# Kernel optimization log

Hardware: AMD Instinct MI355X
Metric: run time of the kernel (lower is better)

Reference implementation:

```python
import jax, jax.numpy as jnp
import numpy as np

NODELEN = 17949
N_NODES = 512
N_EDGES = 4096
H2 = 768
EMB = 128
IN_DIM = 2 * NODELEN


def _seg_mean(h, src, dst, n):
    # gather neighbor features and mean-reduce per destination node
    msg = h[src]                                   # [E, F]
    s = jax.ops.segment_sum(msg, dst, num_segments=n)
    deg = jax.ops.segment_sum(jnp.ones((src.shape[0],), h.dtype), dst, num_segments=n)
    return s / jnp.maximum(deg, 1.0)[:, None]


def setup_inputs() -> dict:
    key = jax.random.key(0)
    ks = jax.random.split(key, 12)
    s = 0.02
    return {
        "x": jax.random.normal(ks[0], (N_NODES, NODELEN), jnp.float32),
        "edge_src": jax.random.randint(ks[1], (N_EDGES,), 0, N_NODES),
        "edge_dst": jax.random.randint(ks[2], (N_EDGES,), 0, N_NODES),
        "W_e2": jax.random.normal(ks[3], (H2, IN_DIM), jnp.float32) * s,
        "b_e2": jnp.zeros((H2,), jnp.float32),
        "W_e3": jax.random.normal(ks[4], (EMB, H2), jnp.float32) * s,
        "b_e3": jnp.zeros((EMB,), jnp.float32),
        "W_d1": jax.random.normal(ks[5], (H2, EMB), jnp.float32) * s,
        "b_d1": jnp.zeros((H2,), jnp.float32),
        "W_d3": jax.random.normal(ks[6], (IN_DIM, H2), jnp.float32) * s,
        "b_d3": jnp.zeros((IN_DIM,), jnp.float32),
    }


def reference(x, edge_src, edge_dst, W_e2, b_e2, W_e3, b_e3, W_d1, b_d1, W_d3, b_d3):
    n = x.shape[0]
    # depth-2 recursive GraphSAGE mean aggregation; agg[0]=0 after each hop
    h1 = _seg_mean(x, edge_src, edge_dst, n).at[:, 0].set(0.0)
    h2 = _seg_mean(h1, edge_src, edge_dst, n).at[:, 0].set(0.0)
    emb = jnp.concatenate([x, h2], axis=1)           # [N, 2*NODELEN]
    emb = emb.at[:, 0].set(0.0).at[:, NODELEN].set(0.0)
    # AutoEncoder (eval mode: dropout is identity)
    h = jax.nn.relu(emb @ W_e2.T + b_e2)
    encoded = h @ W_e3.T + b_e3
    h = jax.nn.relu(encoded @ W_d1.T + b_d1)
    decoded = h @ W_d3.T + b_d3
    return encoded, decoded
```

## Files before the change

kernel.cpp:

```cpp
#include <hip/hip_runtime.h>
#include <hip/hip_bf16.h>

#define NODELEN 17949
#define NN 512
#define NE 4096
#define H2 768
#define EMB 128
#define IN_DIM (2 * NODELEN)
#define KP1 35904
#define KITERS1 561
#define SPLITS 24
#define KCHUNK1 24
#define FPAD 18048
#define RPAD4 35968

#define BM 128
#define BN 128
#define BK 64

typedef __bf16 bf16x8 __attribute__((ext_vector_type(8)));
typedef float f32x4 __attribute__((ext_vector_type(4)));

#define GPTR(p) ((const __attribute__((address_space(1))) void*)(p))
#define LPTR(p) ((__attribute__((address_space(3))) void*)(p))


__global__ void k_zero_int(int* p, int n) {
    int i = blockIdx.x * 256 + threadIdx.x;
    if (i < n) p[i] = 0;
}

__global__ void k_zero_f4(float4* p, int n4) {
    int i = blockIdx.x * 256 + threadIdx.x;
    if (i < n4) p[i] = make_float4(0.f, 0.f, 0.f, 0.f);
}

__global__ void k_deg(const int* __restrict__ dst, int* __restrict__ cnt) {
    int e = blockIdx.x * 256 + threadIdx.x;
    if (e < NE) atomicAdd(&cnt[dst[e]], 1);
}

__global__ void k_invdeg(const int* __restrict__ cnt, float* __restrict__ invdeg) {
    int i = blockIdx.x * 256 + threadIdx.x;
    if (i < NN) {
        int c = cnt[i];
        invdeg[i] = 1.0f / (float)(c > 1 ? c : 1);
    }
}

__global__ void k_scatter(const int* __restrict__ src, const int* __restrict__ dst,
                          const float* __restrict__ invdeg, float* __restrict__ A) {
    int e = blockIdx.x * 256 + threadIdx.x;
    if (e < NE) {
        int d = dst[e];
        atomicAdd(&A[(size_t)d * NN + src[e]], invdeg[d]);
    }
}

__global__ void k_a2(const float* __restrict__ A, __bf16* __restrict__ A2b) {
    int i = blockIdx.x;
    int t = threadIdx.x;
    __shared__ float row[NN];
    row[t] = A[(size_t)i * NN + t];
    row[t + 256] = A[(size_t)i * NN + 256 + t];
    __syncthreads();
    float a0 = 0.f, a1 = 0.f;
    for (int s = 0; s < NN; ++s) {
        float a = row[s];
        if (a != 0.f) {
            a0 += a * A[(size_t)s * NN + t];
            a1 += a * A[(size_t)s * NN + 256 + t];
        }
    }
    A2b[(size_t)i * NN + t] = (__bf16)a0;
    A2b[(size_t)i * NN + 256 + t] = (__bf16)a1;
}

__global__ void k_xt_emb(const float* __restrict__ x, __bf16* __restrict__ xT,
                         __bf16* __restrict__ embb) {
    __shared__ float t[64][65];
    int f0 = blockIdx.x * 64, s0 = blockIdx.y * 64;
    int tx = threadIdx.x & 63, ty = threadIdx.x >> 6;
#pragma unroll
    for (int r = 0; r < 16; ++r) {
        int f = f0 + tx;
        int s = s0 + ty * 16 + r;
        float v = (f < NODELEN) ? x[(size_t)s * NODELEN + f] : 0.f;
        t[ty * 16 + r][tx] = v;
        if (f < NODELEN)
            embb[(size_t)s * KP1 + f] = (__bf16)((f == 0) ? 0.f : v);
    }
    __syncthreads();
#pragma unroll
    for (int r = 0; r < 16; ++r) {
        int f = f0 + ty * 16 + r;
        if (f < FPAD) xT[(size_t)f * NN + s0 + tx] = (__bf16)t[tx][ty * 16 + r];
    }
}

__global__ void k_pad(__bf16* __restrict__ embb) {
    int i = blockIdx.x * 256 + threadIdx.x;
    const int PAD = KP1 - IN_DIM;
    if (i < NN * PAD) {
        int n = i / PAD, c = i % PAD;
        embb[(size_t)n * KP1 + IN_DIM + c] = (__bf16)0.f;
    }
}

__global__ void k_cvt(const float* __restrict__ src, __bf16* __restrict__ dst,
                      int R, int C, int Rpad, int Cpad) {
    int C8 = Cpad / 8;
    int idx = blockIdx.x * 256 + threadIdx.x;
    if (idx >= Rpad * C8) return;
    int r = idx / C8, c8 = (idx % C8) * 8;
    __align__(16) __bf16 o[8];
    if (r < R && c8 + 8 <= C) {
        const float2* p = (const float2*)(src + (size_t)r * C + c8);
#pragma unroll
        for (int j = 0; j < 4; ++j) {
            float2 f = p[j];
            o[2 * j] = (__bf16)f.x;
            o[2 * j + 1] = (__bf16)f.y;
        }
    } else {
#pragma unroll
        for (int j = 0; j < 8; ++j) {
            int c = c8 + j;
            o[j] = (r < R && c < C) ? (__bf16)src[(size_t)r * C + c] : (__bf16)0.f;
        }
    }
    *(uint4*)&dst[(size_t)r * Cpad + c8] = *(uint4*)o;
}


template <int EPI>
__global__ __launch_bounds__(256, 4) void gemm_k(
        const __bf16* __restrict__ A, int lda,
        const __bf16* __restrict__ B, int ldb,
        int Nvalid, int kIters, int kChunk,
        float* __restrict__ Cf, int ldc, const float* __restrict__ bias,
        __bf16* __restrict__ Cb) {
    __shared__ __align__(16) __bf16 As[BM * BK];
    __shared__ __align__(16) __bf16 Bs[BN * BK];

    const int tid = threadIdx.x;

    const int gx = gridDim.x, gy = gridDim.y;
    const int nwg = gx * gy * (int)gridDim.z;
    const int fid = blockIdx.x + gx * (blockIdx.y + gy * blockIdx.z);
    const int q = nwg >> 3, r = nwg & 7;
    const int xcd = fid & 7, idx = fid >> 3;
    const int lid = (xcd < r) ? xcd * (q + 1) + idx
                              : r * (q + 1) + (xcd - r) * q + idx;
    const int m0 = (lid % gx) * BM;
    const int rem = lid / gx;
    const int n0 = (rem % gy) * BN;
    const int z = rem / gy;

    int it0 = z * kChunk;
    int it1 = it0 + kChunk;
    if (it1 > kIters) it1 = kIters;

    const int wave = tid >> 6;
    const int lane = tid & 63;
    const int wm = (wave & 1) * 64;
    const int wn = (wave >> 1) * 64;
    const int fl = lane & 15;
    const int fq = lane >> 4;

    const __bf16* Abase = A + (size_t)(m0 + (tid >> 3)) * lda + (tid & 7) * 8;
    const __bf16* Bbase = B + (size_t)(n0 + (tid >> 3)) * ldb + (tid & 7) * 8;
    char* AsW = (char*)As + wave * 1024;
    char* BsW = (char*)Bs + wave * 1024;

    f32x4 acc[4][4] = {};

    for (int it = it0; it < it1; ++it) {
        const __bf16* Ag = Abase + it * BK;
        const __bf16* Bg = Bbase + it * BK;
#pragma unroll
        for (int rr = 0; rr < 4; ++rr)
            __builtin_amdgcn_global_load_lds(
                GPTR(Ag + (size_t)rr * 32 * lda), LPTR(AsW + rr * 4096), 16, 0, 0);
#pragma unroll
        for (int rr = 0; rr < 4; ++rr)
            __builtin_amdgcn_global_load_lds(
                GPTR(Bg + (size_t)rr * 32 * ldb), LPTR(BsW + rr * 4096), 16, 0, 0);
        __syncthreads();

#pragma unroll
        for (int ks = 0; ks < 2; ++ks) {
            const int kk = ks * 32 + fq * 8;
            bf16x8 af[4], bfr[4];
#pragma unroll
            for (int i = 0; i < 4; ++i)
                af[i] = *(const bf16x8*)&As[(wm + i * 16 + fl) * BK + kk];
#pragma unroll
            for (int j = 0; j < 4; ++j)
                bfr[j] = *(const bf16x8*)&Bs[(wn + j * 16 + fl) * BK + kk];
#pragma unroll
            for (int i = 0; i < 4; ++i)
#pragma unroll
                for (int j = 0; j < 4; ++j)
                    acc[i][j] = __builtin_amdgcn_mfma_f32_16x16x32_bf16(
                        af[i], bfr[j], acc[i][j], 0, 0, 0);
        }
        __syncthreads();
    }

#pragma unroll
    for (int i = 0; i < 4; ++i) {
#pragma unroll
        for (int j = 0; j < 4; ++j) {
#pragma unroll
            for (int rr = 0; rr < 4; ++rr) {
                int m = m0 + wm + i * 16 + fq * 4 + rr;
                int n = n0 + wn + j * 16 + fl;
                float v = acc[i][j][rr];
                if (EPI == 0) {
                    Cf[((size_t)z * NN + m) * H2 + n] = v;
                } else if (EPI == 1) {
                    if (n < Nvalid) Cf[(size_t)m * ldc + n] = v + bias[n];
                } else {
                    if (n < Nvalid)
                        Cb[(size_t)m * KP1 + NODELEN + n] = (n == 0) ? (__bf16)0.f : (__bf16)v;
                }
            }
        }
    }
}

__global__ void k_reduce(const float* __restrict__ partials,
                         const float* __restrict__ bias, float* __restrict__ h) {
    const int T4 = NN * H2 / 4;
    int i4 = blockIdx.x * 256 + threadIdx.x;
    if (i4 >= T4) return;
    const float4* p = (const float4*)partials;
    float4 s = make_float4(0.f, 0.f, 0.f, 0.f);
#pragma unroll
    for (int zz = 0; zz < SPLITS; ++zz) {
        float4 v = p[(size_t)zz * T4 + i4];
        s.x += v.x; s.y += v.y; s.z += v.z; s.w += v.w;
    }
    const float4 b = *(const float4*)&bias[(i4 * 4) % H2];
    s.x += b.x; s.y += b.y; s.z += b.z; s.w += b.w;
    s.x = s.x > 0.f ? s.x : 0.f;
    s.y = s.y > 0.f ? s.y : 0.f;
    s.z = s.z > 0.f ? s.z : 0.f;
    s.w = s.w > 0.f ? s.w : 0.f;
    *(float4*)&h[(size_t)i4 * 4] = s;
}

__global__ void k_enc(const float* __restrict__ h, const float* __restrict__ W,
                      const float* __restrict__ b, float* __restrict__ out) {
    int m = blockIdx.x, e = threadIdx.x;
    const float4* hr = (const float4*)(h + (size_t)m * H2);
    const float4* wr = (const float4*)(W + (size_t)e * H2);
    float s = 0.f;
#pragma unroll 4
    for (int i = 0; i < H2 / 4; ++i) {
        float4 a = hr[i];
        float4 w = wr[i];
        s += a.x * w.x + a.y * w.y + a.z * w.z + a.w * w.w;
    }
    out[(size_t)m * EMB + e] = s + b[e];
}

__global__ void k_dec1(const float* __restrict__ enc, const float* __restrict__ W,
                       const float* __restrict__ b, __bf16* __restrict__ hd) {
    int m = blockIdx.x;
    __shared__ float er[EMB];
    if (threadIdx.x < EMB) er[threadIdx.x] = enc[(size_t)m * EMB + threadIdx.x];
    __syncthreads();
    for (int j = threadIdx.x; j < H2; j += 256) {
        const float4* wr = (const float4*)(W + (size_t)j * EMB);
        float s = 0.f;
#pragma unroll
        for (int i = 0; i < EMB / 4; ++i) {
            float4 w = wr[i];
            s += w.x * er[4 * i] + w.y * er[4 * i + 1] + w.z * er[4 * i + 2] +
                 w.w * er[4 * i + 3];
        }
        float v = s + b[j];
        hd[(size_t)m * H2 + j] = (__bf16)(v > 0.f ? v : 0.f);
    }
}


extern "C" void kernel_launch(void* const* d_in, const int* in_sizes, int n_in,
                              void* d_out, int out_size, void* d_ws, size_t ws_size,
                              hipStream_t stream) {
    const float* x = (const float*)d_in[0];
    const int* esrc = (const int*)d_in[1];
    const int* edst = (const int*)d_in[2];
    const float* W_e2 = (const float*)d_in[3];
    const float* b_e2 = (const float*)d_in[4];
    const float* W_e3 = (const float*)d_in[5];
    const float* b_e3 = (const float*)d_in[6];
    const float* W_d1 = (const float*)d_in[7];
    const float* b_d1 = (const float*)d_in[8];
    const float* W_d3 = (const float*)d_in[9];
    const float* b_d3 = (const float*)d_in[10];
    float* out = (float*)d_out;

    char* w = (char*)d_ws;
    auto alloc = [&](size_t bytes) {
        char* p = w;
        w += (bytes + 255) & ~(size_t)255;
        return p;
    };
    __bf16* embb = (__bf16*)alloc((size_t)NN * KP1 * 2);
    char* uni = (char*)alloc((size_t)SPLITS * NN * H2 * 4);
    __bf16* xTb = (__bf16*)uni;
    float* Adj = (float*)(uni + (size_t)FPAD * NN * 2);
    __bf16* A2b = (__bf16*)((char*)Adj + (size_t)NN * NN * 4);
    int* cnt = (int*)((char*)A2b + (size_t)NN * NN * 2);
    float* invdeg = (float*)((char*)cnt + 2048);
    float* partials = (float*)uni;
    char* Wbig = alloc((size_t)RPAD4 * H2 * 2);
    __bf16* We2b = (__bf16*)Wbig;
    __bf16* Wd3b = (__bf16*)Wbig;
    float* h = (float*)alloc((size_t)NN * H2 * 4);
    __bf16* hd_b = (__bf16*)alloc((size_t)NN * H2 * 2);

    k_zero_int<<<2, 256, 0, stream>>>(cnt, NN);
    k_zero_f4<<<256, 256, 0, stream>>>((float4*)Adj, NN * NN / 4);
    k_deg<<<NE / 256, 256, 0, stream>>>(edst, cnt);
    k_invdeg<<<2, 256, 0, stream>>>(cnt, invdeg);
    k_scatter<<<NE / 256, 256, 0, stream>>>(esrc, edst, invdeg, Adj);
    k_a2<<<NN, 256, 0, stream>>>(Adj, A2b);

    dim3 gxt(FPAD / 64, NN / 64);
    k_xt_emb<<<gxt, 256, 0, stream>>>(x, xTb, embb);
    k_pad<<<(NN * (KP1 - IN_DIM) + 255) / 256, 256, 0, stream>>>(embb);

    dim3 gh2(NN / BM, FPAD / BN, 1);
    gemm_k<2><<<gh2, 256, 0, stream>>>(
        A2b, NN, xTb, NN, NODELEN, NN / BK, NN / BK,
        (float*)nullptr, 0, (const float*)nullptr, embb);

    k_cvt<<<(H2 * (KP1 / 8) + 255) / 256, 256, 0, stream>>>(
        W_e2, We2b, H2, IN_DIM, H2, KP1);

    dim3 g1(NN / BM, H2 / BN, SPLITS);
    gemm_k<0><<<g1, 256, 0, stream>>>(
        embb, KP1, We2b, KP1, H2, KITERS1, KCHUNK1,
        partials, 0, (const float*)nullptr, (__bf16*)nullptr);

    k_cvt<<<(RPAD4 * (H2 / 8) + 255) / 256, 256, 0, stream>>>(
        W_d3, Wd3b, IN_DIM, H2, RPAD4, H2);

    k_reduce<<<(NN * H2 / 4 + 255) / 256, 256, 0, stream>>>(partials, b_e2, h);

    k_enc<<<NN, EMB, 0, stream>>>(h, W_e3, b_e3, out);

    k_dec1<<<NN, 256, 0, stream>>>(out, W_d1, b_d1, hd_b);

    dim3 g4(NN / BM, RPAD4 / BN, 1);
    gemm_k<1><<<g4, 256, 0, stream>>>(
        hd_b, H2, Wd3b, H2, IN_DIM, H2 / BK, H2 / BK,
        out + (size_t)NN * EMB, IN_DIM, b_d3, (__bf16*)nullptr);
}
```

Before: 545.4 us.

## Fuse fp32-to-bf16 weight conversion into GEMM B-tile loads

Measured after the change: 599.4 us. 9.9% more time.

```diff
diff --git a/kernel.cpp b/kernel.cpp
--- a/kernel.cpp
+++ b/kernel.cpp
@@ -107,37 +107,12 @@
     }
 }
 
-__global__ void k_cvt(const float* __restrict__ src, __bf16* __restrict__ dst,
-                      int R, int C, int Rpad, int Cpad) {
-    int C8 = Cpad / 8;
-    int idx = blockIdx.x * 256 + threadIdx.x;
-    if (idx >= Rpad * C8) return;
-    int r = idx / C8, c8 = (idx % C8) * 8;
-    __align__(16) __bf16 o[8];
-    if (r < R && c8 + 8 <= C) {
-        const float2* p = (const float2*)(src + (size_t)r * C + c8);
-#pragma unroll
-        for (int j = 0; j < 4; ++j) {
-            float2 f = p[j];
-            o[2 * j] = (__bf16)f.x;
-            o[2 * j + 1] = (__bf16)f.y;
-        }
-    } else {
-#pragma unroll
-        for (int j = 0; j < 8; ++j) {
-            int c = c8 + j;
-            o[j] = (r < R && c < C) ? (__bf16)src[(size_t)r * C + c] : (__bf16)0.f;
-        }
-    }
-    *(uint4*)&dst[(size_t)r * Cpad + c8] = *(uint4*)o;
-}
-
-
-template <int EPI>
-__global__ __launch_bounds__(256, 4) void gemm_k(
+
+template <int EPI, bool BF32>
+__device__ __forceinline__ void gemm_body(
         const __bf16* __restrict__ A, int lda,
-        const __bf16* __restrict__ B, int ldb,
-        int Nvalid, int kIters, int kChunk,
+        const void* __restrict__ Bv, int ldb,
+        int Nvalid, int Brows, int Kvalid, int kIters, int kChunk,
         float* __restrict__ Cf, int ldc, const float* __restrict__ bias,
         __bf16* __restrict__ Cb) {
     __shared__ __align__(16) __bf16 As[BM * BK];
@@ -169,23 +144,54 @@
     const int fq = lane >> 4;
 
     const __bf16* Abase = A + (size_t)(m0 + (tid >> 3)) * lda + (tid & 7) * 8;
-    const __bf16* Bbase = B + (size_t)(n0 + (tid >> 3)) * ldb + (tid & 7) * 8;
     char* AsW = (char*)As + wave * 1024;
+    const __bf16* Bbase_h = (const __bf16*)Bv + (size_t)(n0 + (tid >> 3)) * ldb + (tid & 7) * 8;
     char* BsW = (char*)Bs + wave * 1024;
+    const float* Bf = (const float*)Bv;
+    const int btrow = n0 + (tid >> 3);
+    const int bkoff = (tid & 7) * 8;
 
     f32x4 acc[4][4] = {};
 
     for (int it = it0; it < it1; ++it) {
-        const __bf16* Ag = Abase + it * BK;
-        const __bf16* Bg = Bbase + it * BK;
+        const int k0 = it * BK;
+        const __bf16* Ag = Abase + k0;
 #pragma unroll
         for (int rr = 0; rr < 4; ++rr)
             __builtin_amdgcn_global_load_lds(
                 GPTR(Ag + (size_t)rr * 32 * lda), LPTR(AsW + rr * 4096), 16, 0, 0);
-#pragma unroll
-        for (int rr = 0; rr < 4; ++rr)
-            __builtin_amdgcn_global_load_lds(
-                GPTR(Bg + (size_t)rr * 32 * ldb), LPTR(BsW + rr * 4096), 16, 0, 0);
+        if (BF32) {
+#pragma unroll
+            for (int rr = 0; rr < 4; ++rr) {
+                const int brow = btrow + rr * 32;
+                const int kc = k0 + bkoff;
+                const float* Bg = Bf + (size_t)brow * ldb + kc;
+                float4 f0, f1;
+                if (brow < Brows && kc + 8 <= Kvalid) {
+                    f0 = ((const float4*)Bg)[0];
+                    f1 = ((const float4*)Bg)[1];
+                } else {
+                    float tv[8];
+#pragma unroll
+                    for (int j = 0; j < 8; ++j)
+                        tv[j] = (brow < Brows && kc + j < Kvalid) ? Bg[j] : 0.f;
+                    f0 = make_float4(tv[0], tv[1], tv[2], tv[3]);
+                    f1 = make_float4(tv[4], tv[5], tv[6], tv[7]);
+                }
+                __align__(16) __bf16 o[8];
+                o[0] = (__bf16)f0.x; o[1] = (__bf16)f0.y;
+                o[2] = (__bf16)f0.z; o[3] = (__bf16)f0.w;
+                o[4] = (__bf16)f1.x; o[5] = (__bf16)f1.y;
+                o[6] = (__bf16)f1.z; o[7] = (__bf16)f1.w;
+                *(uint4*)((char*)Bs + rr * 4096 + tid * 16) = *(uint4*)o;
+            }
+        } else {
+            const __bf16* Bg = Bbase_h + k0;
+#pragma unroll
+            for (int rr = 0; rr < 4; ++rr)
+                __builtin_amdgcn_global_load_lds(
+                    GPTR(Bg + (size_t)rr * 32 * ldb), LPTR(BsW + rr * 4096), 16, 0, 0);
+        }
         __syncthreads();
 
 #pragma unroll
@@ -228,6 +234,27 @@
             }
         }
     }
+}
+
+__global__ __launch_bounds__(256, 4) void k_gemm_h2(
+        const __bf16* __restrict__ A2b, const __bf16* __restrict__ xTb,
+        __bf16* __restrict__ embb) {
+    gemm_body<2, false>(A2b, NN, xTb, NN, NODELEN, FPAD, NN, NN / BK, NN / BK,
+                        (float*)nullptr, 0, (const float*)nullptr, embb);
+}
+
+__global__ __launch_bounds__(256, 4) void k_gemm_e2(
+        const __bf16* __restrict__ embb, const float* __restrict__ We2,
+        float* __restrict__ partials) {
+    gemm_body<0, true>(embb, KP1, We2, IN_DIM, H2, H2, IN_DIM, KITERS1, KCHUNK1,
+                       partials, 0, (const float*)nullptr, (__bf16*)nullptr);
+}
+
+__global__ __launch_bounds__(256, 4) void k_gemm_d3(
+        const __bf16* __restrict__ hd_b, const float* __restrict__ Wd3,
+        const float* __restrict__ b_d3, float* __restrict__ dec) {
+    gemm_body<1, true>(hd_b, H2, Wd3, H2, IN_DIM, IN_DIM, H2, H2 / BK, H2 / BK,
+                       dec, IN_DIM, b_d3, (__bf16*)nullptr);
 }
 
 __global__ void k_reduce(const float* __restrict__ partials,
@@ -317,9 +344,6 @@
     int* cnt = (int*)((char*)A2b + (size_t)NN * NN * 2);
     float* invdeg = (float*)((char*)cnt + 2048);
     float* partials = (float*)uni;
-    char* Wbig = alloc((size_t)RPAD4 * H2 * 2);
-    __bf16* We2b = (__bf16*)Wbig;
-    __bf16* Wd3b = (__bf16*)Wbig;
     float* h = (float*)alloc((size_t)NN * H2 * 4);
     __bf16* hd_b = (__bf16*)alloc((size_t)NN * H2 * 2);
 
@@ -335,20 +359,10 @@
     k_pad<<<(NN * (KP1 - IN_DIM) + 255) / 256, 256, 0, stream>>>(embb);
 
     dim3 gh2(NN / BM, FPAD / BN, 1);
-    gemm_k<2><<<gh2, 256, 0, stream>>>(
-        A2b, NN, xTb, NN, NODELEN, NN / BK, NN / BK,
-        (float*)nullptr, 0, (const float*)nullptr, embb);
-
-    k_cvt<<<(H2 * (KP1 / 8) + 255) / 256, 256, 0, stream>>>(
-        W_e2, We2b, H2, IN_DIM, H2, KP1);
+    k_gemm_h2<<<gh2, 256, 0, stream>>>(A2b, xTb, embb);
 
     dim3 g1(NN / BM, H2 / BN, SPLITS);
-    gemm_k<0><<<g1, 256, 0, stream>>>(
-        embb, KP1, We2b, KP1, H2, KITERS1, KCHUNK1,
-        partials, 0, (const float*)nullptr, (__bf16*)nullptr);
-
-    k_cvt<<<(RPAD4 * (H2 / 8) + 255) / 256, 256, 0, stream>>>(
-        W_d3, Wd3b, IN_DIM, H2, RPAD4, H2);
+    k_gemm_e2<<<g1, 256, 0, stream>>>(embb, W_e2, partials);
 
     k_reduce<<<(NN * H2 / 4 + 255) / 256, 256, 0, stream>>>(partials, b_e2, h);
 
@@ -357,7 +371,5 @@
     k_dec1<<<NN, 256, 0, stream>>>(out, W_d1, b_d1, hd_b);
 
     dim3 g4(NN / BM, RPAD4 / BN, 1);
-    gemm_k<1><<<g4, 256, 0, stream>>>(
-        hd_b, H2, Wd3b, H2, IN_DIM, H2 / BK, H2 / BK,
-        out + (size_t)NN * EMB, IN_DIM, b_d3, (__bf16*)nullptr);
-}
+    k_gemm_d3<<<g4, 256, 0, stream>>>(hd_b, W_d3, b_d3, out + (size_t)NN * EMB);
+}
```
